# Kernel optimization log

Measured on AMD Instinct MI355X. Metric: run time of the kernel, lower is better.

Reference implementation:

```python
import jax, jax.numpy as jnp
import numpy as np

HID = 1024   # hidden_size
NH = 16      # num_heads
NKV = 4      # num_kv_heads
HD = 64      # head_dim
C = 64       # chunk_size
RATIO = 0.125  # freq_cutoff_ratio
KS = 7       # conv_kernel_size


def setup_inputs() -> dict:
    key = jax.random.key(0)
    ks = jax.random.split(key, 11)
    B, N = 4, 4096
    s = 0.02
    return {
        "hidden_states": jax.random.normal(ks[0], (B, N, HID), jnp.float32),
        "q_w": jax.random.normal(ks[1], (NH * HD, HID), jnp.float32) * s,
        "k_w": jax.random.normal(ks[2], (NKV * HD, HID), jnp.float32) * s,
        "v_w": jax.random.normal(ks[3], (NKV * HD, HID), jnp.float32) * s,
        "o_w": jax.random.normal(ks[4], (HID, NH * HD), jnp.float32) * s,
        "dw_r": jax.random.normal(ks[5], (HID, 1, KS), jnp.float32) * 0.3,
        "pw_r": jax.random.normal(ks[6], (HID, HID), jnp.float32) * s,
        "dw_i": jax.random.normal(ks[7], (HID, 1, KS), jnp.float32) * 0.3,
        "pw_i": jax.random.normal(ks[8], (HID, HID), jnp.float32) * s,
        "gate_w": jax.random.normal(ks[9], (HID, HID), jnp.float32) * s,
        "alpha_raw": jnp.zeros((1,), jnp.float32),
    }


def _block_causal_attention(x, qw, kw, vw, ow, k):
    # x: [B, nc, k, D] real. Flatten chunk freq bins; chunk j attends to chunks 0..j.
    B, nc, _, D = x.shape
    T = nc * k
    xf = x.reshape(B, T, D)
    q = (xf @ qw.T).reshape(B, T, NH, HD).transpose(0, 2, 1, 3)    # [B,H,T,hd]
    kk = (xf @ kw.T).reshape(B, T, NKV, HD).transpose(0, 2, 1, 3)
    v = (xf @ vw.T).reshape(B, T, NKV, HD).transpose(0, 2, 1, 3)
    rep = NH // NKV
    kk = jnp.repeat(kk, rep, axis=1)
    v = jnp.repeat(v, rep, axis=1)
    chunk_ids = jnp.arange(T) // k
    mask = chunk_ids[:, None] >= chunk_ids[None, :]                # [T,T] bool
    scores = jnp.einsum('bhqd,bhkd->bhqk', q, kk) / np.float32(np.sqrt(HD))
    scores = jnp.where(mask[None, None], scores, jnp.finfo(scores.dtype).min)
    p = jax.nn.softmax(scores, axis=-1)
    o = jnp.einsum('bhqk,bhkd->bhqd', p, v)
    o = o.transpose(0, 2, 1, 3).reshape(B, T, NH * HD)
    return (o @ ow.T).reshape(B, nc, k, D)


def _causal_conv(x, dw, pw):
    # x: [B, nc, L, D] real. Depthwise causal conv + GELU + pointwise conv.
    B, nc, L, D = x.shape
    xc = x.reshape(B * nc, L, D).transpose(0, 2, 1)                # [BN, D, L]
    xp = jnp.pad(xc, ((0, 0), (0, 0), (KS - 1, 0)))                # causal left pad
    y = jax.lax.conv_general_dilated(
        xp, dw, window_strides=(1,), padding='VALID',
        dimension_numbers=('NCH', 'OIH', 'NCH'), feature_group_count=D)
    y = jax.nn.gelu(y, approximate=False)
    y = jnp.einsum('ncl,oc->nol', y, pw)                           # 1x1 conv
    return y.transpose(0, 2, 1).reshape(B, nc, L, D)


def _forward(hidden_states, q_w, k_w, v_w, o_w, dw_r, pw_r, dw_i, pw_i, gate_w, alpha_raw):
    B, N, D = hidden_states.shape
    pad_len = (-N) % C
    x = jnp.pad(hidden_states, ((0, 0), (0, pad_len), (0, 0))) if pad_len else hidden_states
    nc = x.shape[1] // C
    chunks = x.reshape(B, nc, C, D)
    Xh = jnp.fft.rfft(chunks.astype(jnp.float32), axis=2)          # [B,nc,M,D] complex
    M = Xh.shape[2]
    k = max(1, int(M * RATIO))
    X_low, X_high = Xh[:, :, :k, :], Xh[:, :, k:, :]
    # low-freq: block-causal attention on real and imag parts separately
    A_r = _block_causal_attention(X_low.real, q_w, k_w, v_w, o_w, k)
    A_i = _block_causal_attention(X_low.imag, q_w, k_w, v_w, o_w, k)
    A_low = jax.lax.complex(A_r, A_i)
    # high-freq: causal conv branch, gated by per-chunk time-domain mean
    H_r = _causal_conv(X_high.real, dw_r, pw_r)
    H_i = _causal_conv(X_high.imag, dw_i, pw_i)
    g = jax.nn.sigmoid(chunks.mean(axis=2) @ gate_w.T)[:, :, None, :]  # [B,nc,1,D]
    A_high = jax.lax.complex(H_r * g, H_i * g) + X_high
    alpha = jax.nn.sigmoid(alpha_raw)                               # [1]
    A_low_fused = alpha * A_low + (1.0 - alpha) * X_low
    Y_hat = jnp.concatenate([A_low_fused, A_high], axis=2)
    Y = jnp.fft.irfft(Y_hat, n=C, axis=2)
    return Y.reshape(B, -1, D)[:, :N, :].astype(hidden_states.dtype)


def reference(hidden_states, q_w, k_w, v_w, o_w, dw_r, pw_r, dw_i, pw_i, gate_w, alpha_raw):
    return _forward(hidden_states, q_w, k_w, v_w, o_w, dw_r, pw_r, dw_i, pw_i, gate_w, alpha_raw)
```

## Files before the change

kernel.cpp:

```cpp
#include <hip/hip_runtime.h>
#include <math.h>


typedef __bf16 bf16_t;
typedef bf16_t bf16x8 __attribute__((ext_vector_type(8)));
typedef float f32x4 __attribute__((ext_vector_type(4)));

#define EP_NONE 0
#define EP_SIGMOID 1
#define EP_FUSELOW 2
#define EP_HIGH 3

__device__ __forceinline__ void gld_lds16(const bf16_t* g, bf16_t* l) {
  __builtin_amdgcn_global_load_lds(
      (const __attribute__((address_space(1))) unsigned int*)g,
      (__attribute__((address_space(3))) unsigned int*)l, 16, 0, 0);
}

__global__ __launch_bounds__(256) void concat_w(const float* __restrict__ qw,
                                                const float* __restrict__ kw,
                                                const float* __restrict__ vw,
                                                bf16_t* __restrict__ W) {
  int i = blockIdx.x * 256 + threadIdx.x;
  float4 v;
  if (i < 262144) v = ((const float4*)qw)[i];
  else if (i < 327680) v = ((const float4*)kw)[i - 262144];
  else v = ((const float4*)vw)[i - 327680];
  bf16_t* o = W + (long)i * 4;
  o[0] = (bf16_t)v.x; o[1] = (bf16_t)v.y; o[2] = (bf16_t)v.z; o[3] = (bf16_t)v.w;
}

__global__ __launch_bounds__(256) void cvt4_bf16(const float* __restrict__ s0,
                                                 const float* __restrict__ s1,
                                                 const float* __restrict__ s2,
                                                 const float* __restrict__ s3,
                                                 bf16_t* __restrict__ d0,
                                                 bf16_t* __restrict__ d1,
                                                 bf16_t* __restrict__ d2,
                                                 bf16_t* __restrict__ d3) {
  int i = blockIdx.x * 256 + threadIdx.x;
  const float* s = blockIdx.y == 0 ? s0 : blockIdx.y == 1 ? s1 : blockIdx.y == 2 ? s2 : s3;
  bf16_t* dst = blockIdx.y == 0 ? d0 : blockIdx.y == 1 ? d1 : blockIdx.y == 2 ? d2 : d3;
  float4 v = ((const float4*)s)[i];
  bf16_t* o = dst + (long)i * 4;
  o[0] = (bf16_t)v.x; o[1] = (bf16_t)v.y; o[2] = (bf16_t)v.z; o[3] = (bf16_t)v.w;
}

__global__ __launch_bounds__(256) void mk_basis(bf16_t* __restrict__ dhi,
                                                bf16_t* __restrict__ dres,
                                                bf16_t* __restrict__ bhi,
                                                bf16_t* __restrict__ bres,
                                                float* __restrict__ tlow) {
  int idx = blockIdx.x * 256 + threadIdx.x;
  const float TW = 6.283185307179586f / 64.f;
  if (idx < 5120) {
    int r = idx >> 6, k = idx & 63;
    float v = 0.f;
    if (r < 33) {
      v = cosf(TW * (float)((r * k) & 63));
    } else if (r < 66) {
      v = -sinf(TW * (float)(((r - 33) * k) & 63));
    }
    bf16_t h = (bf16_t)v;
    float res = v - (float)h;
    int addr = r * 64 + (((k >> 3) ^ (r & 7)) << 3) + (k & 7);
    dhi[addr] = h;
    dres[addr] = (bf16_t)res;
  } else if (idx < 9216) {
    int i = idx - 5120;
    int t = i >> 6, k = i & 63;
    float v = 0.f;
    if (k < 28) {
      int ft = ((4 + k) * t) & 63;
      v = 2.f * cosf(TW * (float)ft) * (1.f / 64.f);
    } else if (k == 28) {
      int ft = (32 * t) & 63;
      v = cosf(TW * (float)ft) * (1.f / 64.f);
    } else if (k < 57) {
      int ft = ((k - 25) * t) & 63;
      v = -2.f * sinf(TW * (float)ft) * (1.f / 64.f);
    }
    bf16_t h = (bf16_t)v;
    float res = v - (float)h;
    int addr = t * 64 + (((k >> 3) ^ (t & 7)) << 3) + (k & 7);
    bhi[addr] = h;
    bres[addr] = (bf16_t)res;
  } else if (idx < 9728) {
    int i = idx - 9216;
    int t = i >> 3, j = i & 7;
    float v = 0.f;
    if (j == 0) v = 1.f / 64.f;
    else if (j < 7) {
      int f = (j + 1) >> 1;
      int ft = (f * t) & 63;
      float th = TW * (float)ft;
      v = (j & 1) ? 2.f * cosf(th) * (1.f / 64.f)
                  : -2.f * sinf(th) * (1.f / 64.f);
    }
    tlow[i] = v;
  }
}

__global__ __launch_bounds__(256) void dft_mfma(
    const float* __restrict__ X, const bf16_t* __restrict__ dhi,
    const bf16_t* __restrict__ dres, bf16_t* __restrict__ Xh,
    bf16_t* __restrict__ XLr, bf16_t* __restrict__ XLi,
    bf16_t* __restrict__ gmean) {
  const int bc = blockIdx.y;
  const int d0 = blockIdx.x * 256;
  const int tid = threadIdx.x;
  const int lane = tid & 63, wave = tid >> 6;
  const int mr = lane & 15, q = lane >> 4;
  const int wn = wave * 64;

  __shared__ bf16_t Ahi[80 * 64];
  __shared__ bf16_t Ares[80 * 64];
  __shared__ bf16_t Bh[256 * 64];
  __shared__ bf16_t Br[256 * 64];

  for (int i = wave; i < 10; i += 4) {
    gld_lds16(dhi + (i * 64 + lane) * 8, Ahi + i * 512);
    gld_lds16(dres + (i * 64 + lane) * 8, Ares + i * 512);
  }

  {
    const float* xc = X + ((long)bc * 64) * 1024 + d0 + tid;
    const int sw = tid & 7;
#pragma unroll
    for (int g = 0; g < 8; g++) {
      bf16x8 vh, vr;
#pragma unroll
      for (int i = 0; i < 8; i++) {
        float v = xc[(long)(g * 8 + i) * 1024];
        bf16_t h = (bf16_t)v;
        vh[i] = h;
        vr[i] = (bf16_t)(v - (float)h);
      }
      *(bf16x8*)&Bh[tid * 64 + ((g ^ sw) << 3)] = vh;
      *(bf16x8*)&Br[tid * 64 + ((g ^ sw) << 3)] = vr;
    }
  }
  __syncthreads();

  f32x4 acc[5][4];
#pragma unroll
  for (int i = 0; i < 5; i++)
#pragma unroll
    for (int j = 0; j < 4; j++) acc[i][j] = (f32x4){0.f, 0.f, 0.f, 0.f};

#pragma unroll
  for (int s = 0; s < 2; s++) {
    bf16x8 bh[4], br[4];
#pragma unroll
    for (int ni = 0; ni < 4; ni++) {
      int dcol = wn + ni * 16 + mr;
      int so = (((s * 4 + q) ^ (dcol & 7)) << 3);
      bh[ni] = *(const bf16x8*)&Bh[dcol * 64 + so];
      br[ni] = *(const bf16x8*)&Br[dcol * 64 + so];
    }
#pragma unroll
    for (int mi = 0; mi < 5; mi++) {
      int trow = mi * 16 + mr;
      int so = (((s * 4 + q) ^ (trow & 7)) << 3);
      bf16x8 ah = *(const bf16x8*)&Ahi[trow * 64 + so];
      bf16x8 ar = *(const bf16x8*)&Ares[trow * 64 + so];
#pragma unroll
      for (int ni = 0; ni < 4; ni++) {
        acc[mi][ni] = __builtin_amdgcn_mfma_f32_16x16x32_bf16(
            ah, bh[ni], acc[mi][ni], 0, 0, 0);
        acc[mi][ni] = __builtin_amdgcn_mfma_f32_16x16x32_bf16(
            ah, br[ni], acc[mi][ni], 0, 0, 0);
        acc[mi][ni] = __builtin_amdgcn_mfma_f32_16x16x32_bf16(
            ar, bh[ni], acc[mi][ni], 0, 0, 0);
      }
    }
  }

  const int b = bc >> 6, ch = bc & 63;
  bf16_t* xp = Xh + (long)bc * 66 * 1024 + d0;
#pragma unroll
  for (int mi = 0; mi < 5; mi++) {
#pragma unroll
    for (int r = 0; r < 4; r++) {
      int row = mi * 16 + q * 4 + r;
      if (row >= 66) continue;
#pragma unroll
      for (int ni = 0; ni < 4; ni++) {
        int col = wn + ni * 16 + mr;
        float val = acc[mi][ni][r];
        xp[(long)row * 1024 + col] = (bf16_t)val;
        if (row == 0)
          gmean[(long)bc * 1024 + d0 + col] = (bf16_t)(val * (1.f / 64.f));
        if (row < 4)
          XLr[((long)(b * 256 + ch * 4 + row)) * 1024 + d0 + col] = (bf16_t)val;
        if (row >= 33 && row < 37)
          XLi[((long)(b * 256 + ch * 4 + row - 33)) * 1024 + d0 + col] =
              (bf16_t)val;
      }
    }
  }
}

template <int EMODE>
__global__ __launch_bounds__(256) void mmbf_kernel(
    const bf16_t* __restrict__ A0, const bf16_t* __restrict__ A1,
    const bf16_t* __restrict__ B0, const bf16_t* __restrict__ B1,
    int N, int K,
    void* __restrict__ C0v, void* __restrict__ C1v,
    const bf16_t* __restrict__ E0, const bf16_t* __restrict__ E1,
    bf16_t* __restrict__ XhMut,
    const float* __restrict__ gate, const float* __restrict__ alpha_ptr) {
  constexpr int BM = 128, BN = 128, BK = 32;
  __shared__ bf16_t As[BM * BK];
  __shared__ bf16_t Bs[BN * BK];
  const int z = blockIdx.z;
  const bf16_t* A = z ? A1 : A0;
  const bf16_t* B = z ? B1 : B0;
  void* Cv = z ? C1v : C0v;
  const bf16_t* E = z ? E1 : E0;
  const int imoff = z ? 33 * 1024 : 0;
  const int tid = threadIdx.x;
  const int lane = tid & 63;
  const int wave = tid >> 6;
  const int wm = (wave & 1) * 64, wn = (wave >> 1) * 64;
  const int m0 = blockIdx.x * BM, n0 = blockIdx.y * BN;
  const int q = lane >> 4, mr = lane & 15;
  const int lrow = lane >> 2, lk8 = (lane & 3) * 8;

  f32x4 acc[4][4];
#pragma unroll
  for (int i = 0; i < 4; i++)
#pragma unroll
    for (int j = 0; j < 4; j++) acc[i][j] = (f32x4){0.f, 0.f, 0.f, 0.f};

  const long arow0 = (long)(m0 + wave * 16 + lrow) * K + lk8;
  const long brow0 = (long)(n0 + wave * 16 + lrow) * K + lk8;

  for (int kb = 0; kb < K; kb += BK) {
#pragma unroll
    for (int it = 0; it < 2; it++) {
      gld_lds16(A + arow0 + (long)it * 64 * K + kb, As + (wave * 16 + it * 64) * BK);
      gld_lds16(B + brow0 + (long)it * 64 * K + kb, Bs + (wave * 16 + it * 64) * BK);
    }
    __syncthreads();
    bf16x8 af[4], bfr[4];
#pragma unroll
    for (int mi = 0; mi < 4; mi++)
      af[mi] = *(const bf16x8*)&As[(wm + mi * 16 + mr) * BK + q * 8];
#pragma unroll
    for (int ni = 0; ni < 4; ni++)
      bfr[ni] = *(const bf16x8*)&Bs[(wn + ni * 16 + mr) * BK + q * 8];
#pragma unroll
    for (int mi = 0; mi < 4; mi++)
#pragma unroll
      for (int ni = 0; ni < 4; ni++)
        acc[mi][ni] = __builtin_amdgcn_mfma_f32_16x16x32_bf16(
            af[mi], bfr[ni], acc[mi][ni], 0, 0, 0);
    __syncthreads();
  }

  float alpha = 0.f;
  if constexpr (EMODE == EP_FUSELOW) alpha = 1.f / (1.f + __expf(-alpha_ptr[0]));
#pragma unroll
  for (int mi = 0; mi < 4; mi++) {
#pragma unroll
    for (int ni = 0; ni < 4; ni++) {
      int col = n0 + wn + ni * 16 + mr;
      int rbase = m0 + wm + mi * 16 + q * 4;
#pragma unroll
      for (int r = 0; r < 4; r++) {
        int row = rbase + r;
        float val = acc[mi][ni][r];
        if constexpr (EMODE == EP_NONE) {
          ((bf16_t*)Cv)[(long)row * N + col] = (bf16_t)val;
        } else if constexpr (EMODE == EP_SIGMOID) {
          ((float*)Cv)[(long)row * N + col] = 1.f / (1.f + __expf(-val));
        } else if constexpr (EMODE == EP_FUSELOW) {
          float xl = (float)E[(long)row * 1024 + col];
          ((float*)Cv)[(long)row * 1024 + col] = alpha * val + (1.f - alpha) * xl;
        } else {
          int bc = row / 29, l = row - bc * 29;
          long x = ((long)bc * 66 + 4 + l) * 1024 + imoff + col;
          XhMut[x] = (bf16_t)fmaf(val, gate[(long)bc * 1024 + col], (float)XhMut[x]);
        }
      }
    }
  }
}

__global__ __launch_bounds__(512, 2) void gemm256_high(
    const bf16_t* __restrict__ A0, const bf16_t* __restrict__ A1,
    const bf16_t* __restrict__ B0, const bf16_t* __restrict__ B1,
    bf16_t* __restrict__ XhMut, const float* __restrict__ gate) {
  constexpr int K = 1024;
  constexpr int NT = K / 32;
  __shared__ bf16_t lds[4][2][256 * 32];

  const int id = blockIdx.x;
  const int kk = (id & 7) * 29 + (id >> 3);
  const int mt = kk >> 3, rem = kk & 7;
  const int nt = rem & 3, z = rem >> 2;
  const bf16_t* A = z ? A1 : A0;
  const bf16_t* B = z ? B1 : B0;
  const int imoff = z ? 33 * 1024 : 0;
  const int m0 = mt * 256, n0 = nt * 256;

  const int tid = threadIdx.x;
  const int lane = tid & 63, wave = tid >> 6;
  const int wm = (wave & 1) * 128, wn = (wave >> 1) * 64;
  const int q = lane >> 4, mr = lane & 15;
  const int srow = tid >> 2;
  const int gk8 = (((tid & 3) ^ ((((tid >> 2) & 3) + ((tid >> 4) & 3)) & 3)) << 3);

  f32x4 acc[8][4];
#pragma unroll
  for (int i = 0; i < 8; i++)
#pragma unroll
    for (int j = 0; j < 4; j++) acc[i][j] = (f32x4){0.f, 0.f, 0.f, 0.f};

  auto stage = [&](int t) {
    const int bi = t & 3;
    const int kb = t * 32;
#pragma unroll
    for (int rd = 0; rd < 2; rd++) {
      gld_lds16(A + (long)(m0 + rd * 128 + srow) * K + kb + gk8,
                &lds[bi][0][(rd * 512 + wave * 64) * 8]);
      gld_lds16(B + (long)(n0 + rd * 128 + srow) * K + kb + gk8,
                &lds[bi][1][(rd * 512 + wave * 64) * 8]);
    }
  };

  stage(0);
  stage(1);
  stage(2);

  const int asl = (q ^ (((mr & 3) + ((mr >> 2) & 3)) & 3)) * 8;

  for (int t = 0; t < NT; t++) {
    if (t < NT - 2)
      asm volatile("s_waitcnt vmcnt(8)" ::: "memory");
    else if (t == NT - 2)
      asm volatile("s_waitcnt vmcnt(4)" ::: "memory");
    else
      asm volatile("s_waitcnt vmcnt(0)" ::: "memory");
    __builtin_amdgcn_sched_barrier(0);
    __builtin_amdgcn_s_barrier();
    if (t + 3 < NT) stage(t + 3);

    const bf16_t* As_ = &lds[t & 3][0][0];
    const bf16_t* Bs_ = &lds[t & 3][1][0];
    bf16x8 bfr[4];
#pragma unroll
    for (int ni = 0; ni < 4; ni++)
      bfr[ni] = *(const bf16x8*)&Bs_[(wn + ni * 16 + mr) * 32 + asl];
    __builtin_amdgcn_s_setprio(1);
#pragma unroll
    for (int mi = 0; mi < 8; mi++) {
      bf16x8 af = *(const bf16x8*)&As_[(wm + mi * 16 + mr) * 32 + asl];
#pragma unroll
      for (int ni = 0; ni < 4; ni++)
        acc[mi][ni] = __builtin_amdgcn_mfma_f32_16x16x32_bf16(
            af, bfr[ni], acc[mi][ni], 0, 0, 0);
    }
    __builtin_amdgcn_s_setprio(0);
  }

#pragma unroll
  for (int mi = 0; mi < 8; mi++) {
#pragma unroll
    for (int r = 0; r < 4; r++) {
      int row = m0 + wm + mi * 16 + q * 4 + r;
      int bc = row / 29, l = row - bc * 29;
      long xbase = ((long)bc * 66 + 4 + l) * 1024 + imoff;
      const float* gp = gate + (long)bc * 1024;
#pragma unroll
      for (int ni = 0; ni < 4; ni++) {
        int col = n0 + wn + ni * 16 + mr;
        long x = xbase + col;
        XhMut[x] = (bf16_t)fmaf(acc[mi][ni][r], gp[col], (float)XhMut[x]);
      }
    }
  }
}

__global__ __launch_bounds__(256) void attn_mfma(const bf16_t* __restrict__ QKVr,
                                                 const bf16_t* __restrict__ QKVi,
                                                 bf16_t* __restrict__ Or_,
                                                 bf16_t* __restrict__ Oi_) {
  const int h = blockIdx.x;
  const int b = blockIdx.y >> 2, qt = blockIdx.y & 3;
  const bf16_t* QKV = blockIdx.z ? QKVi : QKVr;
  bf16_t* O = blockIdx.z ? Oi_ : Or_;
  const int kvh = h >> 2;
  const int tid = threadIdx.x;
  const int lane = tid & 63, wave = tid >> 6;
  const int mr = lane & 15, q4 = lane >> 4;

  __shared__ bf16_t Ks[64 * 72];
  __shared__ bf16_t Vt[64 * 72];
  __shared__ bf16_t Ps[4][16 * 72];

  bf16x8 af[2];
  {
    const bf16_t* qp =
        QKV + (long)(b * 256 + qt * 64 + wave * 16 + mr) * 1536 + h * 64;
    af[0] = *(const bf16x8*)(qp + q4 * 8);
    af[1] = *(const bf16x8*)(qp + 32 + q4 * 8);
  }
  f32x4 Oacc[4];
#pragma unroll
  for (int ni = 0; ni < 4; ni++) Oacc[ni] = (f32x4){0.f, 0.f, 0.f, 0.f};
  float mrow[4], lrow[4];
#pragma unroll
  for (int r = 0; r < 4; r++) { mrow[r] = -1e30f; lrow[r] = 0.f; }

  for (int kt = 0; kt <= qt; kt++) {
#pragma unroll
    for (int it = 0; it < 2; it++) {
      int idx = tid + it * 256;
      int key = idx >> 3, dg = idx & 7;
      const bf16_t* kp = QKV + (long)(b * 256 + kt * 64 + key) * 1536 + 1024 +
                         kvh * 64 + dg * 8;
      *(bf16x8*)&Ks[key * 72 + dg * 8] = *(const bf16x8*)kp;
      bf16x8 vv = *(const bf16x8*)(kp + 256);
#pragma unroll
      for (int j = 0; j < 8; j++) Vt[(dg * 8 + j) * 72 + key] = vv[j];
    }
    __syncthreads();

    f32x4 S[4];
#pragma unroll
    for (int ni = 0; ni < 4; ni++) {
      S[ni] = (f32x4){0.f, 0.f, 0.f, 0.f};
#pragma unroll
      for (int s = 0; s < 2; s++) {
        bf16x8 kb = *(const bf16x8*)&Ks[(ni * 16 + mr) * 72 + s * 32 + q4 * 8];
        S[ni] = __builtin_amdgcn_mfma_f32_16x16x32_bf16(af[s], kb, S[ni], 0, 0, 0);
      }
    }
#pragma unroll
    for (int ni = 0; ni < 4; ni++) {
#pragma unroll
      for (int r = 0; r < 4; r++) {
        float v = S[ni][r] * 0.125f;
        if (kt == qt) {
          int qrow = wave * 16 + q4 * 4 + r;
          int kcol = ni * 16 + mr;
          if ((qrow >> 2) < (kcol >> 2)) v = -1e30f;
        }
        S[ni][r] = v;
      }
    }
#pragma unroll
    for (int r = 0; r < 4; r++) {
      float mx = fmaxf(fmaxf(S[0][r], S[1][r]), fmaxf(S[2][r], S[3][r]));
#pragma unroll
      for (int off = 1; off < 16; off <<= 1) mx = fmaxf(mx, __shfl_xor(mx, off));
      float mn = fmaxf(mrow[r], mx);
      float sc = __expf(mrow[r] - mn);
      mrow[r] = mn;
      float rs = 0.f;
#pragma unroll
      for (int ni = 0; ni < 4; ni++) {
        float p = __expf(S[ni][r] - mn);
        rs += p;
        Ps[wave][(q4 * 4 + r) * 72 + ni * 16 + mr] = (bf16_t)p;
      }
#pragma unroll
      for (int off = 1; off < 16; off <<= 1) rs += __shfl_xor(rs, off);
      lrow[r] = lrow[r] * sc + rs;
#pragma unroll
      for (int ni = 0; ni < 4; ni++) Oacc[ni][r] *= sc;
    }
    bf16x8 pa[2];
    pa[0] = *(const bf16x8*)&Ps[wave][mr * 72 + q4 * 8];
    pa[1] = *(const bf16x8*)&Ps[wave][mr * 72 + 32 + q4 * 8];
#pragma unroll
    for (int ni = 0; ni < 4; ni++) {
#pragma unroll
      for (int s = 0; s < 2; s++) {
        bf16x8 vb = *(const bf16x8*)&Vt[(ni * 16 + mr) * 72 + s * 32 + q4 * 8];
        Oacc[ni] = __builtin_amdgcn_mfma_f32_16x16x32_bf16(pa[s], vb, Oacc[ni], 0, 0, 0);
      }
    }
    __syncthreads();
  }

#pragma unroll
  for (int r = 0; r < 4; r++) {
    float inv = 1.f / lrow[r];
    long row = b * 256 + qt * 64 + wave * 16 + q4 * 4 + r;
#pragma unroll
    for (int ni = 0; ni < 4; ni++)
      O[row * 1024 + h * 64 + ni * 16 + mr] = (bf16_t)(Oacc[ni][r] * inv);
  }
}

__global__ __launch_bounds__(256) void dwconv_kernel(const bf16_t* __restrict__ Xh,
                                                     const float* __restrict__ dwr,
                                                     const float* __restrict__ dwi,
                                                     bf16_t* __restrict__ Gr,
                                                     bf16_t* __restrict__ Gi) {
  const int d = blockIdx.x * 256 + threadIdx.x;
  const int bc = blockIdx.y;
  const float* dw = blockIdx.z ? dwi : dwr;
  bf16_t* G = blockIdx.z ? Gi : Gr;
  const int imoff = blockIdx.z ? 33 * 1024 : 0;
  float w[7];
#pragma unroll
  for (int j = 0; j < 7; j++) w[j] = dw[d * 7 + j];
  float x[29];
#pragma unroll
  for (int l = 0; l < 29; l++)
    x[l] = (float)Xh[((long)bc * 66 + 4 + l) * 1024 + imoff + d];
#pragma unroll
  for (int l = 0; l < 29; l++) {
    float y = 0.f;
#pragma unroll
    for (int j = 0; j < 7; j++) {
      int src = l - 6 + j;
      if (src >= 0) y = fmaf(w[j], x[src], y);
    }
    float ge = 0.5f * y * (1.f + erff(y * 0.7071067811865475f));
    G[((long)bc * 29 + l) * 1024 + d] = (bf16_t)ge;
  }
}

__global__ __launch_bounds__(256) void irfft_mfma(
    const bf16_t* __restrict__ Xh, const float* __restrict__ Afr,
    const float* __restrict__ Afi, const bf16_t* __restrict__ bhi,
    const bf16_t* __restrict__ bres, const float* __restrict__ tlow,
    float* __restrict__ out) {
  const int bc = blockIdx.y;
  const int d0 = blockIdx.x * 256;
  const int tid = threadIdx.x;
  const int lane = tid & 63, wave = tid >> 6;
  const int mr = lane & 15, q = lane >> 4;
  const int wn = wave * 64;

  __shared__ bf16_t Ahi[64 * 64];
  __shared__ bf16_t Ares[64 * 64];
  __shared__ bf16_t Bs[256 * 64];
  __shared__ float Tl[64 * 8];

  gld_lds16(bhi + (wave * 64 + lane) * 8, Ahi + wave * 64 * 8);
  gld_lds16(bhi + (256 + wave * 64 + lane) * 8, Ahi + (256 + wave * 64) * 8);
  gld_lds16(bres + (wave * 64 + lane) * 8, Ares + wave * 64 * 8);
  gld_lds16(bres + (256 + wave * 64 + lane) * 8, Ares + (256 + wave * 64) * 8);
  if (tid < 128) ((float4*)Tl)[tid] = ((const float4*)tlow)[tid];

  {
    const bf16_t* xc = Xh + (long)bc * 66 * 1024 + d0 + tid;
    const int sw = tid & 7;
#pragma unroll
    for (int g = 0; g < 8; g++) {
      bf16x8 v;
#pragma unroll
      for (int i = 0; i < 8; i++) {
        int j = g * 8 + i;
        int row = (j < 29) ? (4 + j) : (8 + j);
        v[i] = (j < 57) ? xc[(long)row * 1024] : (bf16_t)0.f;
      }
      *(bf16x8*)&Bs[tid * 64 + ((g ^ sw) << 3)] = v;
    }
  }
  __syncthreads();

  f32x4 acc[4][4];
#pragma unroll
  for (int i = 0; i < 4; i++)
#pragma unroll
    for (int j = 0; j < 4; j++) acc[i][j] = (f32x4){0.f, 0.f, 0.f, 0.f};

#pragma unroll
  for (int s = 0; s < 2; s++) {
    bf16x8 bfv[4];
#pragma unroll
    for (int ni = 0; ni < 4; ni++) {
      int dcol = wn + ni * 16 + mr;
      bfv[ni] = *(const bf16x8*)&Bs[dcol * 64 + (((s * 4 + q) ^ (dcol & 7)) << 3)];
    }
#pragma unroll
    for (int mi = 0; mi < 4; mi++) {
      int trow = mi * 16 + mr;
      int so = (((s * 4 + q) ^ (trow & 7)) << 3);
      bf16x8 ah = *(const bf16x8*)&Ahi[trow * 64 + so];
      bf16x8 ar = *(const bf16x8*)&Ares[trow * 64 + so];
#pragma unroll
      for (int ni = 0; ni < 4; ni++) {
        acc[mi][ni] = __builtin_amdgcn_mfma_f32_16x16x32_bf16(
            ah, bfv[ni], acc[mi][ni], 0, 0, 0);
        acc[mi][ni] = __builtin_amdgcn_mfma_f32_16x16x32_bf16(
            ar, bfv[ni], acc[mi][ni], 0, 0, 0);
      }
    }
  }

  const int arow = (bc >> 6) * 256 + (bc & 63) * 4;
  float R[4][7];
#pragma unroll
  for (int ni = 0; ni < 4; ni++) {
    long ab = (long)arow * 1024 + d0 + wn + ni * 16 + mr;
    R[ni][0] = Afr[ab];
    R[ni][1] = Afr[ab + 1024];
    R[ni][2] = Afi[ab + 1024];
    R[ni][3] = Afr[ab + 2048];
    R[ni][4] = Afi[ab + 2048];
    R[ni][5] = Afr[ab + 3072];
    R[ni][6] = Afi[ab + 3072];
  }
  const long obase = ((long)bc * 64) * 1024 + d0;
#pragma unroll
  for (int mi = 0; mi < 4; mi++) {
#pragma unroll
    for (int r = 0; r < 4; r++) {
      int t = mi * 16 + q * 4 + r;
      const float* tl = &Tl[t * 8];
#pragma unroll
      for (int ni = 0; ni < 4; ni++) {
        float low = tl[0] * R[ni][0];
        low = fmaf(tl[1], R[ni][1], low);
        low = fmaf(tl[2], R[ni][2], low);
        low = fmaf(tl[3], R[ni][3], low);
        low = fmaf(tl[4], R[ni][4], low);
        low = fmaf(tl[5], R[ni][5], low);
        low = fmaf(tl[6], R[ni][6], low);
        out[obase + (long)t * 1024 + wn + ni * 16 + mr] = acc[mi][ni][r] + low;
      }
    }
  }
}

extern "C" void kernel_launch(void* const* d_in, const int* in_sizes, int n_in,
                              void* d_out, int out_size, void* d_ws, size_t ws_size,
                              hipStream_t stream) {
  const float* hidden = (const float*)d_in[0];
  const float* q_w = (const float*)d_in[1];
  const float* k_w = (const float*)d_in[2];
  const float* v_w = (const float*)d_in[3];
  const float* o_w = (const float*)d_in[4];
  const float* dw_r = (const float*)d_in[5];
  const float* pw_r = (const float*)d_in[6];
  const float* dw_i = (const float*)d_in[7];
  const float* pw_i = (const float*)d_in[8];
  const float* gate_w = (const float*)d_in[9];
  const float* alpha_raw = (const float*)d_in[10];
  float* out = (float*)d_out;

  float* ws = (float*)d_ws;
  float* Afr = ws;
  float* Afi = Afr + 1048576;
  float* gg = Afi + 1048576;
  bf16_t* bws = (bf16_t*)(gg + 262144);
  bf16_t* Xh = bws;
  bf16_t* Wqkv_b = Xh + 17301504;
  bf16_t* ow_b = Wqkv_b + 1572864;
  bf16_t* gw_b = ow_b + 1048576;
  bf16_t* pwr_b = gw_b + 1048576;
  bf16_t* pwi_b = pwr_b + 1048576;
  bf16_t* XLr = pwi_b + 1048576;
  bf16_t* XLi = XLr + 1048576;
  bf16_t* gmean = XLi + 1048576;
  bf16_t* QKVbr = gmean + 262144;
  bf16_t* QKVbi = QKVbr + 1572864;
  bf16_t* Obr = QKVbi + 1572864;
  bf16_t* Obi = Obr + 1048576;
  bf16_t* Gr = Obi + 1048576;
  bf16_t* Gi = Gr + 7602176;
  bf16_t* bhi = Gi + 7602176;
  bf16_t* bres = bhi + 4096;
  bf16_t* dbhi = bres + 4096;
  bf16_t* dbres = dbhi + 5120;
  float* tlowp = (float*)(dbres + 5120);

  mk_basis<<<38, 256, 0, stream>>>(dbhi, dbres, bhi, bres, tlowp);
  dft_mfma<<<dim3(4, 256), 256, 0, stream>>>(hidden, dbhi, dbres, Xh, XLr,
                                             XLi, gmean);
  concat_w<<<1536, 256, 0, stream>>>(q_w, k_w, v_w, Wqkv_b);
  cvt4_bf16<<<dim3(1024, 4), 256, 0, stream>>>(o_w, gate_w, pw_r, pw_i,
                                               ow_b, gw_b, pwr_b, pwi_b);
  mmbf_kernel<EP_NONE><<<dim3(8, 12, 2), 256, 0, stream>>>(
      XLr, XLi, Wqkv_b, Wqkv_b, 1536, 1024, QKVbr, QKVbi, nullptr, nullptr,
      nullptr, nullptr, nullptr);
  mmbf_kernel<EP_SIGMOID><<<dim3(2, 8, 1), 256, 0, stream>>>(
      gmean, gmean, gw_b, gw_b, 1024, 1024, gg, gg, nullptr, nullptr,
      nullptr, nullptr, nullptr);
  attn_mfma<<<dim3(16, 16, 2), 256, 0, stream>>>(QKVbr, QKVbi, Obr, Obi);
  mmbf_kernel<EP_FUSELOW><<<dim3(8, 8, 2), 256, 0, stream>>>(
      Obr, Obi, ow_b, ow_b, 1024, 1024, Afr, Afi, XLr, XLi,
      nullptr, nullptr, alpha_raw);
  dwconv_kernel<<<dim3(4, 256, 2), 256, 0, stream>>>(Xh, dw_r, dw_i, Gr, Gi);
  gemm256_high<<<dim3(232), 512, 0, stream>>>(Gr, Gi, pwr_b, pwi_b, Xh, gg);
  irfft_mfma<<<dim3(4, 256), 256, 0, stream>>>(Xh, Afr, Afi, bhi, bres,
                                               tlowp, out);
}
```

Baseline: 343.6 us.

## Unify GEMMs into pipelined 128-tile kernel, merge weight prep, halve DFT blocks

Replaces the simple synchronous mmbf GEMM and the 256-tile high-frequency GEMM with a single 128x128 GEMM template. The template uses a 4-deep LDS ring of global_load_lds stages, vmcnt-based waits, setprio around the MFMAs, and an XCD-aware tile remap. It also merges the two weight conversion kernels into one launch. The DFT and iDFT kernels drop from 256 to 128 threads per block to double the block count. The goal is to hide load latency and add parallelism, but the high-frequency GEMM loses its larger tile and LDS swizzle, which may raise memory traffic and bank conflicts.

```diff
diff --git a/kernel.cpp b/kernel.cpp
--- a/kernel.cpp
+++ b/kernel.cpp
@@ -17,32 +17,29 @@
       (__attribute__((address_space(3))) unsigned int*)l, 16, 0, 0);
 }
 
-__global__ __launch_bounds__(256) void concat_w(const float* __restrict__ qw,
-                                                const float* __restrict__ kw,
-                                                const float* __restrict__ vw,
-                                                bf16_t* __restrict__ W) {
-  int i = blockIdx.x * 256 + threadIdx.x;
+__global__ __launch_bounds__(256) void prep_w(
+    const float* __restrict__ qw, const float* __restrict__ kw,
+    const float* __restrict__ vw, const float* __restrict__ ow,
+    const float* __restrict__ gw, const float* __restrict__ pwr,
+    const float* __restrict__ pwi, bf16_t* __restrict__ Wqkv,
+    bf16_t* __restrict__ owb, bf16_t* __restrict__ gwb,
+    bf16_t* __restrict__ pwrb, bf16_t* __restrict__ pwib) {
+  int gi = blockIdx.x * 256 + threadIdx.x;
   float4 v;
-  if (i < 262144) v = ((const float4*)qw)[i];
-  else if (i < 327680) v = ((const float4*)kw)[i - 262144];
-  else v = ((const float4*)vw)[i - 327680];
-  bf16_t* o = W + (long)i * 4;
-  o[0] = (bf16_t)v.x; o[1] = (bf16_t)v.y; o[2] = (bf16_t)v.z; o[3] = (bf16_t)v.w;
-}
-
-__global__ __launch_bounds__(256) void cvt4_bf16(const float* __restrict__ s0,
-                                                 const float* __restrict__ s1,
-                                                 const float* __restrict__ s2,
-                                                 const float* __restrict__ s3,
-                                                 bf16_t* __restrict__ d0,
-                                                 bf16_t* __restrict__ d1,
-                                                 bf16_t* __restrict__ d2,
-                                                 bf16_t* __restrict__ d3) {
-  int i = blockIdx.x * 256 + threadIdx.x;
-  const float* s = blockIdx.y == 0 ? s0 : blockIdx.y == 1 ? s1 : blockIdx.y == 2 ? s2 : s3;
-  bf16_t* dst = blockIdx.y == 0 ? d0 : blockIdx.y == 1 ? d1 : blockIdx.y == 2 ? d2 : d3;
-  float4 v = ((const float4*)s)[i];
-  bf16_t* o = dst + (long)i * 4;
+  bf16_t* o;
+  if (gi < 393216) {
+    if (gi < 262144) v = ((const float4*)qw)[gi];
+    else if (gi < 327680) v = ((const float4*)kw)[gi - 262144];
+    else v = ((const float4*)vw)[gi - 327680];
+    o = Wqkv + (long)gi * 4;
+  } else {
+    int j = gi - 393216;
+    int sel = j >> 18, off = j & 262143;
+    const float* s = sel == 0 ? ow : sel == 1 ? gw : sel == 2 ? pwr : pwi;
+    bf16_t* d = sel == 0 ? owb : sel == 1 ? gwb : sel == 2 ? pwrb : pwib;
+    v = ((const float4*)s)[off];
+    o = d + (long)off * 4;
+  }
   o[0] = (bf16_t)v.x; o[1] = (bf16_t)v.y; o[2] = (bf16_t)v.z; o[3] = (bf16_t)v.w;
 }
 
@@ -101,13 +98,13 @@
   }
 }
 
-__global__ __launch_bounds__(256) void dft_mfma(
+__global__ __launch_bounds__(128) void dft_mfma(
     const float* __restrict__ X, const bf16_t* __restrict__ dhi,
     const bf16_t* __restrict__ dres, bf16_t* __restrict__ Xh,
     bf16_t* __restrict__ XLr, bf16_t* __restrict__ XLi,
     bf16_t* __restrict__ gmean) {
   const int bc = blockIdx.y;
-  const int d0 = blockIdx.x * 256;
+  const int d0 = blockIdx.x * 128;
   const int tid = threadIdx.x;
   const int lane = tid & 63, wave = tid >> 6;
   const int mr = lane & 15, q = lane >> 4;
@@ -115,10 +112,10 @@
 
   __shared__ bf16_t Ahi[80 * 64];
   __shared__ bf16_t Ares[80 * 64];
-  __shared__ bf16_t Bh[256 * 64];
-  __shared__ bf16_t Br[256 * 64];
-
-  for (int i = wave; i < 10; i += 4) {
+  __shared__ bf16_t Bh[128 * 64];
+  __shared__ bf16_t Br[128 * 64];
+
+  for (int i = wave; i < 10; i += 2) {
     gld_lds16(dhi + (i * 64 + lane) * 8, Ahi + i * 512);
     gld_lds16(dres + (i * 64 + lane) * 8, Ares + i * 512);
   }
@@ -202,30 +199,35 @@
 }
 
 template <int EMODE>
-__global__ __launch_bounds__(256) void mmbf_kernel(
+__global__ __launch_bounds__(256, 2) void gemm128(
     const bf16_t* __restrict__ A0, const bf16_t* __restrict__ A1,
     const bf16_t* __restrict__ B0, const bf16_t* __restrict__ B1,
-    int N, int K,
+    int N, int ntc, int zc,
     void* __restrict__ C0v, void* __restrict__ C1v,
     const bf16_t* __restrict__ E0, const bf16_t* __restrict__ E1,
     bf16_t* __restrict__ XhMut,
     const float* __restrict__ gate, const float* __restrict__ alpha_ptr) {
-  constexpr int BM = 128, BN = 128, BK = 32;
-  __shared__ bf16_t As[BM * BK];
-  __shared__ bf16_t Bs[BN * BK];
-  const int z = blockIdx.z;
+  constexpr int K = 1024;
+  constexpr int NT = 32;
+  __shared__ bf16_t lds[4][2][128 * 32];
+
+  const int nwg = gridDim.x;
+  const int g = (blockIdx.x & 7) * (nwg >> 3) + (blockIdx.x >> 3);
+  const int per_mt = ntc * zc;
+  const int mt = g / per_mt, rem = g - mt * per_mt;
+  const int nt = rem % ntc, z = rem / ntc;
   const bf16_t* A = z ? A1 : A0;
   const bf16_t* B = z ? B1 : B0;
   void* Cv = z ? C1v : C0v;
   const bf16_t* E = z ? E1 : E0;
   const int imoff = z ? 33 * 1024 : 0;
+  const int m0 = mt * 128, n0 = nt * 128;
+
   const int tid = threadIdx.x;
-  const int lane = tid & 63;
-  const int wave = tid >> 6;
+  const int lane = tid & 63, wave = tid >> 6;
   const int wm = (wave & 1) * 64, wn = (wave >> 1) * 64;
-  const int m0 = blockIdx.x * BM, n0 = blockIdx.y * BN;
   const int q = lane >> 4, mr = lane & 15;
-  const int lrow = lane >> 2, lk8 = (lane & 3) * 8;
+  const int srow = tid >> 2, sk8 = (tid & 3) * 8;
 
   f32x4 acc[4][4];
 #pragma unroll
@@ -233,30 +235,49 @@
 #pragma unroll
     for (int j = 0; j < 4; j++) acc[i][j] = (f32x4){0.f, 0.f, 0.f, 0.f};
 
-  const long arow0 = (long)(m0 + wave * 16 + lrow) * K + lk8;
-  const long brow0 = (long)(n0 + wave * 16 + lrow) * K + lk8;
-
-  for (int kb = 0; kb < K; kb += BK) {
+  auto stage = [&](int t) {
+    const int bi = t & 3;
+    const int kb = t * 32;
 #pragma unroll
     for (int it = 0; it < 2; it++) {
-      gld_lds16(A + arow0 + (long)it * 64 * K + kb, As + (wave * 16 + it * 64) * BK);
-      gld_lds16(B + brow0 + (long)it * 64 * K + kb, Bs + (wave * 16 + it * 64) * BK);
-    }
-    __syncthreads();
-    bf16x8 af[4], bfr[4];
-#pragma unroll
-    for (int mi = 0; mi < 4; mi++)
-      af[mi] = *(const bf16x8*)&As[(wm + mi * 16 + mr) * BK + q * 8];
+      gld_lds16(A + (long)(m0 + it * 64 + srow) * K + kb + sk8,
+                &lds[bi][0][(it * 256 + wave * 64) * 8]);
+      gld_lds16(B + (long)(n0 + it * 64 + srow) * K + kb + sk8,
+                &lds[bi][1][(it * 256 + wave * 64) * 8]);
+    }
+  };
+
+  stage(0);
+  stage(1);
+  stage(2);
+
+  for (int t = 0; t < NT; t++) {
+    if (t < NT - 2)
+      asm volatile("s_waitcnt vmcnt(8)" ::: "memory");
+    else if (t == NT - 2)
+      asm volatile("s_waitcnt vmcnt(4)" ::: "memory");
+    else
+      asm volatile("s_waitcnt vmcnt(0)" ::: "memory");
+    __builtin_amdgcn_sched_barrier(0);
+    __builtin_amdgcn_s_barrier();
+    if (t + 3 < NT) stage(t + 3);
+
+    const bf16_t* As_ = &lds[t & 3][0][0];
+    const bf16_t* Bs_ = &lds[t & 3][1][0];
+    bf16x8 bfr[4];
 #pragma unroll
     for (int ni = 0; ni < 4; ni++)
-      bfr[ni] = *(const bf16x8*)&Bs[(wn + ni * 16 + mr) * BK + q * 8];
-#pragma unroll
-    for (int mi = 0; mi < 4; mi++)
+      bfr[ni] = *(const bf16x8*)&Bs_[(wn + ni * 16 + mr) * 32 + q * 8];
+    __builtin_amdgcn_s_setprio(1);
+#pragma unroll
+    for (int mi = 0; mi < 4; mi++) {
+      bf16x8 af = *(const bf16x8*)&As_[(wm + mi * 16 + mr) * 32 + q * 8];
 #pragma unroll
       for (int ni = 0; ni < 4; ni++)
         acc[mi][ni] = __builtin_amdgcn_mfma_f32_16x16x32_bf16(
-            af[mi], bfr[ni], acc[mi][ni], 0, 0, 0);
-    __syncthreads();
+            af, bfr[ni], acc[mi][ni], 0, 0, 0);
+    }
+    __builtin_amdgcn_s_setprio(0);
   }
 
   float alpha = 0.f;
@@ -288,101 +309,6 @@
   }
 }
 
-__global__ __launch_bounds__(512, 2) void gemm256_high(
-    const bf16_t* __restrict__ A0, const bf16_t* __restrict__ A1,
-    const bf16_t* __restrict__ B0, const bf16_t* __restrict__ B1,
-    bf16_t* __restrict__ XhMut, const float* __restrict__ gate) {
-  constexpr int K = 1024;
-  constexpr int NT = K / 32;
-  __shared__ bf16_t lds[4][2][256 * 32];
-
-  const int id = blockIdx.x;
-  const int kk = (id & 7) * 29 + (id >> 3);
-  const int mt = kk >> 3, rem = kk & 7;
-  const int nt = rem & 3, z = rem >> 2;
-  const bf16_t* A = z ? A1 : A0;
-  const bf16_t* B = z ? B1 : B0;
-  const int imoff = z ? 33 * 1024 : 0;
-  const int m0 = mt * 256, n0 = nt * 256;
-
-  const int tid = threadIdx.x;
-  const int lane = tid & 63, wave = tid >> 6;
-  const int wm = (wave & 1) * 128, wn = (wave >> 1) * 64;
-  const int q = lane >> 4, mr = lane & 15;
-  const int srow = tid >> 2;
-  const int gk8 = (((tid & 3) ^ ((((tid >> 2) & 3) + ((tid >> 4) & 3)) & 3)) << 3);
-
-  f32x4 acc[8][4];
-#pragma unroll
-  for (int i = 0; i < 8; i++)
-#pragma unroll
-    for (int j = 0; j < 4; j++) acc[i][j] = (f32x4){0.f, 0.f, 0.f, 0.f};
-
-  auto stage = [&](int t) {
-    const int bi = t & 3;
-    const int kb = t * 32;
-#pragma unroll
-    for (int rd = 0; rd < 2; rd++) {
-      gld_lds16(A + (long)(m0 + rd * 128 + srow) * K + kb + gk8,
-                &lds[bi][0][(rd * 512 + wave * 64) * 8]);
-      gld_lds16(B + (long)(n0 + rd * 128 + srow) * K + kb + gk8,
-                &lds[bi][1][(rd * 512 + wave * 64) * 8]);
-    }
-  };
-
-  stage(0);
-  stage(1);
-  stage(2);
-
-  const int asl = (q ^ (((mr & 3) + ((mr >> 2) & 3)) & 3)) * 8;
-
-  for (int t = 0; t < NT; t++) {
-    if (t < NT - 2)
-      asm volatile("s_waitcnt vmcnt(8)" ::: "memory");
-    else if (t == NT - 2)
-      asm volatile("s_waitcnt vmcnt(4)" ::: "memory");
-    else
-      asm volatile("s_waitcnt vmcnt(0)" ::: "memory");
-    __builtin_amdgcn_sched_barrier(0);
-    __builtin_amdgcn_s_barrier();
-    if (t + 3 < NT) stage(t + 3);
-
-    const bf16_t* As_ = &lds[t & 3][0][0];
-    const bf16_t* Bs_ = &lds[t & 3][1][0];
-    bf16x8 bfr[4];
-#pragma unroll
-    for (int ni = 0; ni < 4; ni++)
-      bfr[ni] = *(const bf16x8*)&Bs_[(wn + ni * 16 + mr) * 32 + asl];
-    __builtin_amdgcn_s_setprio(1);
-#pragma unroll
-    for (int mi = 0; mi < 8; mi++) {
-      bf16x8 af = *(const bf16x8*)&As_[(wm + mi * 16 + mr) * 32 + asl];
-#pragma unroll
-      for (int ni = 0; ni < 4; ni++)
-        acc[mi][ni] = __builtin_amdgcn_mfma_f32_16x16x32_bf16(
-            af, bfr[ni], acc[mi][ni], 0, 0, 0);
-    }
-    __builtin_amdgcn_s_setprio(0);
-  }
-
-#pragma unroll
-  for (int mi = 0; mi < 8; mi++) {
-#pragma unroll
-    for (int r = 0; r < 4; r++) {
-      int row = m0 + wm + mi * 16 + q * 4 + r;
-      int bc = row / 29, l = row - bc * 29;
-      long xbase = ((long)bc * 66 + 4 + l) * 1024 + imoff;
-      const float* gp = gate + (long)bc * 1024;
-#pragma unroll
-      for (int ni = 0; ni < 4; ni++) {
-        int col = n0 + wn + ni * 16 + mr;
-        long x = xbase + col;
-        XhMut[x] = (bf16_t)fmaf(acc[mi][ni][r], gp[col], (float)XhMut[x]);
-      }
-    }
-  }
-}
-
 __global__ __launch_bounds__(256) void attn_mfma(const bf16_t* __restrict__ QKVr,
                                                  const bf16_t* __restrict__ QKVi,
                                                  bf16_t* __restrict__ Or_,
@@ -526,13 +452,13 @@
   }
 }
 
-__global__ __launch_bounds__(256) void irfft_mfma(
+__global__ __launch_bounds__(128) void irfft_mfma(
     const bf16_t* __restrict__ Xh, const float* __restrict__ Afr,
     const float* __restrict__ Afi, const bf16_t* __restrict__ bhi,
     const bf16_t* __restrict__ bres, const float* __restrict__ tlow,
     float* __restrict__ out) {
   const int bc = blockIdx.y;
-  const int d0 = blockIdx.x * 256;
+  const int d0 = blockIdx.x * 128;
   const int tid = threadIdx.x;
   const int lane = tid & 63, wave = tid >> 6;
   const int mr = lane & 15, q = lane >> 4;
@@ -540,14 +466,14 @@
 
   __shared__ bf16_t Ahi[64 * 64];
   __shared__ bf16_t Ares[64 * 64];
-  __shared__ bf16_t Bs[256 * 64];
+  __shared__ bf16_t Bs[128 * 64];
   __shared__ float Tl[64 * 8];
 
-  gld_lds16(bhi + (wave * 64 + lane) * 8, Ahi + wave * 64 * 8);
-  gld_lds16(bhi + (256 + wave * 64 + lane) * 8, Ahi + (256 + wave * 64) * 8);
-  gld_lds16(bres + (wave * 64 + lane) * 8, Ares + wave * 64 * 8);
-  gld_lds16(bres + (256 + wave * 64 + lane) * 8, Ares + (256 + wave * 64) * 8);
-  if (tid < 128) ((float4*)Tl)[tid] = ((const float4*)tlow)[tid];
+  for (int i = wave; i < 8; i += 2) {
+    gld_lds16(bhi + (i * 64 + lane) * 8, Ahi + i * 512);
+    gld_lds16(bres + (i * 64 + lane) * 8, Ares + i * 512);
+  }
+  ((float4*)Tl)[tid] = ((const float4*)tlow)[tid];
 
   {
     const bf16_t* xc = Xh + (long)bc * 66 * 1024 + d0 + tid;
@@ -674,23 +600,24 @@
   float* tlowp = (float*)(dbres + 5120);
 
   mk_basis<<<38, 256, 0, stream>>>(dbhi, dbres, bhi, bres, tlowp);
-  dft_mfma<<<dim3(4, 256), 256, 0, stream>>>(hidden, dbhi, dbres, Xh, XLr,
+  dft_mfma<<<dim3(8, 256), 128, 0, stream>>>(hidden, dbhi, dbres, Xh, XLr,
                                              XLi, gmean);
-  concat_w<<<1536, 256, 0, stream>>>(q_w, k_w, v_w, Wqkv_b);
-  cvt4_bf16<<<dim3(1024, 4), 256, 0, stream>>>(o_w, gate_w, pw_r, pw_i,
-                                               ow_b, gw_b, pwr_b, pwi_b);
-  mmbf_kernel<EP_NONE><<<dim3(8, 12, 2), 256, 0, stream>>>(
-      XLr, XLi, Wqkv_b, Wqkv_b, 1536, 1024, QKVbr, QKVbi, nullptr, nullptr,
+  prep_w<<<5632, 256, 0, stream>>>(q_w, k_w, v_w, o_w, gate_w, pw_r, pw_i,
+                                   Wqkv_b, ow_b, gw_b, pwr_b, pwi_b);
+  gemm128<EP_NONE><<<192, 256, 0, stream>>>(
+      XLr, XLi, Wqkv_b, Wqkv_b, 1536, 12, 2, QKVbr, QKVbi, nullptr, nullptr,
       nullptr, nullptr, nullptr);
-  mmbf_kernel<EP_SIGMOID><<<dim3(2, 8, 1), 256, 0, stream>>>(
-      gmean, gmean, gw_b, gw_b, 1024, 1024, gg, gg, nullptr, nullptr,
+  gemm128<EP_SIGMOID><<<16, 256, 0, stream>>>(
+      gmean, gmean, gw_b, gw_b, 1024, 8, 1, gg, gg, nullptr, nullptr,
       nullptr, nullptr, nullptr);
   attn_mfma<<<dim3(16, 16, 2), 256, 0, stream>>>(QKVbr, QKVbi, Obr, Obi);
-  mmbf_kernel<EP_FUSELOW><<<dim3(8, 8, 2), 256, 0, stream>>>(
-      Obr, Obi, ow_b, ow_b, 1024, 1024, Afr, Afi, XLr, XLi,
+  gemm128<EP_FUSELOW><<<128, 256, 0, stream>>>(
+      Obr, Obi, ow_b, ow_b, 1024, 8, 2, Afr, Afi, XLr, XLi,
       nullptr, nullptr, alpha_raw);
   dwconv_kernel<<<dim3(4, 256, 2), 256, 0, stream>>>(Xh, dw_r, dw_i, Gr, Gi);
-  gemm256_high<<<dim3(232), 512, 0, stream>>>(Gr, Gi, pwr_b, pwi_b, Xh, gg);
-  irfft_mfma<<<dim3(4, 256), 256, 0, stream>>>(Xh, Afr, Afi, bhi, bres,
+  gemm128<EP_HIGH><<<928, 256, 0, stream>>>(
+      Gr, Gi, pwr_b, pwi_b, 1024, 8, 2, nullptr, nullptr, nullptr, nullptr,
+      Xh, gg, nullptr);
+  irfft_mfma<<<dim3(8, 256), 128, 0, stream>>>(Xh, Afr, Afi, bhi, bres,
                                                tlowp, out);
 }
```

Result: faster. 317.8 us (-7.5%).
